# Kernel optimization log

Hardware: AMD Instinct MI355X
Metric: run time of the kernel (lower is better)

The kernel has to match this reference:

```python
import jax, jax.numpy as jnp
import numpy as np

B, N, C, H = 2, 2048, 1024, 16
D = C // H
SCALE = D ** -0.5


def setup_inputs() -> dict:
    key = jax.random.key(0)
    ks = jax.random.split(key, 4)
    s = 0.02
    return {
        "x": jax.random.normal(ks[0], (B, N, C), dtype=jnp.float32),
        "f": jax.random.normal(ks[1], (B, N, C), dtype=jnp.float32),
        "W_qkv": jax.random.normal(ks[2], (C, 3 * C), dtype=jnp.float32) * s,
        "W_proj": jax.random.normal(ks[3], (C, C), dtype=jnp.float32) * s,
        "b_proj": jnp.zeros((C,), dtype=jnp.float32),
    }


def reference(x, f, W_qkv, W_proj, b_proj):
    b, n, c = x.shape
    h, d = H, c // H
    # qkv projection -> (B,N,3,H,D) -> q,k,v each (B,H,N,D)
    qkv = (x @ W_qkv).reshape(b, n, 3, h, d)
    q = jnp.transpose(qkv[:, :, 0], (0, 2, 1, 3))
    k = jnp.transpose(qkv[:, :, 1], (0, 2, 1, 3))
    v = jnp.transpose(qkv[:, :, 2], (0, 2, 1, 3))
    # full NxN scores, faithful to the original manual MHA
    attn = jax.nn.softmax(jnp.einsum("bhqd,bhkd->bhqk", q, k) * SCALE, axis=-1)
    av = jnp.einsum("bhqk,bhkd->bhqd", attn, v)  # (B,H,N,D)
    # pre-residual output branch
    attn2gcn = jnp.transpose(av, (0, 2, 1, 3)).reshape(b, n, c)
    # residual fuse with f (reshaped per-head in torch; equivalent to flat add)
    fused = attn2gcn + f
    out = fused @ W_proj + b_proj
    return (out, attn2gcn)
```

## Files before the change

### kernel.cpp

```cpp
#include <hip/hip_runtime.h>
#include <hip/hip_bf16.h>

#define OUT1_OFF 4194304
#define QSCALE 0.1803368801111204f

typedef __attribute__((ext_vector_type(8))) short bf16x8;
typedef __attribute__((ext_vector_type(4))) float f32x4;

__device__ __forceinline__ unsigned short f2bf(float x) {
    unsigned u = __float_as_uint(x);
    u += 0x7FFFu + ((u >> 16) & 1u);
    return (unsigned short)(u >> 16);
}

__device__ __forceinline__ void gl2lds16(const unsigned short* g, unsigned short* l) {
    __builtin_amdgcn_global_load_lds(
        (const __attribute__((address_space(1))) unsigned int*)g,
        (__attribute__((address_space(3))) unsigned int*)l, 16, 0, 0);
}

__global__ __launch_bounds__(256) void cvt_bf16(const float* __restrict__ s,
                                                unsigned short* __restrict__ d, int n4) {
    int i = blockIdx.x * 256 + threadIdx.x;
    if (i >= n4) return;
    float4 v = reinterpret_cast<const float4*>(s)[i];
    ushort4 o = make_ushort4(f2bf(v.x), f2bf(v.y), f2bf(v.z), f2bf(v.w));
    reinterpret_cast<ushort4*>(d)[i] = o;
}

__global__ __launch_bounds__(256) void cvt_t(const float* __restrict__ in,
                                             unsigned short* __restrict__ out,
                                             int Kd, int Nd) {
    __shared__ float T[64][65];
    const int tid = threadIdx.x;
    const int r0 = blockIdx.y * 64, c0 = blockIdx.x * 64;
    const int tr = tid >> 3, tc = (tid & 7) * 8;
#pragma unroll
    for (int rr = 0; rr < 64; rr += 32) {
        const float4* p = reinterpret_cast<const float4*>(&in[(r0 + tr + rr) * Nd + c0 + tc]);
        float4 v0 = p[0], v1 = p[1];
        T[tr + rr][tc + 0] = v0.x; T[tr + rr][tc + 1] = v0.y;
        T[tr + rr][tc + 2] = v0.z; T[tr + rr][tc + 3] = v0.w;
        T[tr + rr][tc + 4] = v1.x; T[tr + rr][tc + 5] = v1.y;
        T[tr + rr][tc + 6] = v1.z; T[tr + rr][tc + 7] = v1.w;
    }
    __syncthreads();
#pragma unroll
    for (int rr = 0; rr < 64; rr += 32) {
        int orow = tr + rr;
        ushort4 o0 = make_ushort4(f2bf(T[tc + 0][orow]), f2bf(T[tc + 1][orow]),
                                  f2bf(T[tc + 2][orow]), f2bf(T[tc + 3][orow]));
        ushort4 o1 = make_ushort4(f2bf(T[tc + 4][orow]), f2bf(T[tc + 5][orow]),
                                  f2bf(T[tc + 6][orow]), f2bf(T[tc + 7][orow]));
        unsigned short* dst = &out[(c0 + orow) * Kd + r0 + tc];
        *reinterpret_cast<ushort4*>(dst) = o0;
        *reinterpret_cast<ushort4*>(dst + 4) = o1;
    }
}

__global__ __launch_bounds__(256) void gemm_qkv(const unsigned short* __restrict__ A,
                                                const unsigned short* __restrict__ Bt,
                                                unsigned short* __restrict__ qb,
                                                unsigned short* __restrict__ kb,
                                                unsigned short* __restrict__ vtb) {
    __shared__ __align__(16) unsigned short Sh[16384];
    unsigned short* As = Sh;
    unsigned short* Bs = Sh + 8192;
    const int tid = threadIdx.x;
    const int w = tid >> 6, lane = tid & 63, quad = lane >> 4, l15 = lane & 15;
    const int m0 = blockIdx.y * 128, n0 = blockIdx.x * 128;
    const int wm = (w & 1) * 64, wn = (w >> 1) * 64;
    const int sw = (l15 & 7) << 3;
    f32x4 acc[4][4] = {};
    for (int k0 = 0; k0 < 1024; k0 += 64) {
        __syncthreads();
#pragma unroll
        for (int t = 0; t < 4; ++t) {
            int c = t * 256 + tid;
            int row = c >> 3, jg = ((c & 7) ^ (row & 7)) * 8;
            gl2lds16(&A[(m0 + row) * 1024 + k0 + jg], &As[c * 8]);
            gl2lds16(&Bt[(n0 + row) * 1024 + k0 + jg], &Bs[c * 8]);
        }
        __syncthreads();
#pragma unroll
        for (int kk = 0; kk < 2; ++kk) {
            bf16x8 af[4], bfr[4];
#pragma unroll
            for (int i = 0; i < 4; ++i)
                af[i] = *reinterpret_cast<const bf16x8*>(
                    &As[(wm + i * 16 + l15) * 64 + ((((kk * 4 + quad) << 3) ^ sw))]);
#pragma unroll
            for (int j = 0; j < 4; ++j)
                bfr[j] = *reinterpret_cast<const bf16x8*>(
                    &Bs[(wn + j * 16 + l15) * 64 + ((((kk * 4 + quad) << 3) ^ sw))]);
#pragma unroll
            for (int i = 0; i < 4; ++i)
#pragma unroll
                for (int j = 0; j < 4; ++j)
                    acc[i][j] = __builtin_amdgcn_mfma_f32_16x16x32_bf16(af[i], bfr[j], acc[i][j], 0, 0, 0);
        }
    }
    const int nbase = n0 + wn;
    const int t = nbase >> 10;
    __syncthreads();
    if (t < 2) {
#pragma unroll
        for (int j = 0; j < 4; ++j) {
            int n = nbase + j * 16 + l15;
            int h = (n & 1023) >> 6, dd = n & 63;
#pragma unroll
            for (int i = 0; i < 4; ++i)
#pragma unroll
                for (int r = 0; r < 4; ++r) {
                    int m = m0 + wm + i * 16 + quad * 4 + r;
                    int b = m >> 11, tok = m & 2047;
                    float v = acc[i][j][r];
                    if (t == 0) qb[(((b * 16 + h) * 2048) + tok) * 64 + dd] = f2bf(v * QSCALE);
                    else        kb[(((b * 16 + h) * 2048) + tok) * 64 + dd] = f2bf(v);
                }
        }
    } else {
        unsigned short* scr = Sh + w * 4096;
        const int mb = m0 + wm;
        const int b = mb >> 11, kblk = (mb & 2047) >> 6;
        const int h = (nbase & 1023) >> 6;
#pragma unroll
        for (int i = 0; i < 4; ++i) {
            int slot0 = ((i & 2) << 4) | (quad << 3) | ((i & 1) << 2);
#pragma unroll
            for (int j = 0; j < 4; ++j) {
                unsigned short h0 = f2bf(acc[i][j][0]), h1 = f2bf(acc[i][j][1]);
                unsigned short h2 = f2bf(acc[i][j][2]), h3 = f2bf(acc[i][j][3]);
                uint2 pk = make_uint2((unsigned)h0 | ((unsigned)h1 << 16),
                                      (unsigned)h2 | ((unsigned)h3 << 16));
                *reinterpret_cast<uint2*>(&scr[(j * 16 + l15) * 64 + slot0]) = pk;
            }
        }
        asm volatile("s_waitcnt lgkmcnt(0)" ::: "memory");
        unsigned short* vtile = vtb + (((b * 16 + h) * 32) + kblk) * 4096;
#pragma unroll
        for (int p = 0; p < 8; ++p) {
            int idx = (p * 64 + lane) * 8;
            *reinterpret_cast<uint4*>(&vtile[idx]) = *reinterpret_cast<const uint4*>(&scr[idx]);
        }
    }
}

__global__ __launch_bounds__(256) void attn_kernel(const unsigned short* __restrict__ qb,
                                                   const unsigned short* __restrict__ kb,
                                                   const unsigned short* __restrict__ vtb,
                                                   const float* __restrict__ f,
                                                   float* __restrict__ attn2_out,
                                                   unsigned short* __restrict__ fusedb) {
    __shared__ __align__(16) unsigned short Ksw[2][4096];
    __shared__ __align__(16) unsigned short Vsw[2][4096];
    const int tid = threadIdx.x;
    const int w = tid >> 6, lane = tid & 63, quad = lane >> 4, l15 = lane & 15;
    const int bid = blockIdx.x;
    const int qtile = bid >> 5;
    const int bh = (bid & 7) * 4 + ((bid >> 3) & 3);
    const int q0 = qtile * 128 + w * 32;
    const unsigned short* qrl = &qb[(bh * 2048 + q0 + l15) * 64 + quad * 8];
    const unsigned short* qrh = &qb[(bh * 2048 + q0 + 16 + l15) * 64 + quad * 8];
    bf16x8 ql0 = *reinterpret_cast<const bf16x8*>(qrl);
    bf16x8 ql1 = *reinterpret_cast<const bf16x8*>(qrl + 32);
    bf16x8 qh0 = *reinterpret_cast<const bf16x8*>(qrh);
    bf16x8 qh1 = *reinterpret_cast<const bf16x8*>(qrh + 32);
    const unsigned short* kt0 = kb + bh * 131072;
    const unsigned short* vt0 = vtb + bh * 131072;
    const int c1 = tid, c2 = tid + 256;
    const int gu1 = (((c1 & ~7) | ((c1 & 7) ^ ((c1 >> 3) & 7))) << 3);
    const int gu2 = (((c2 & ~7) | ((c2 & 7) ^ ((c2 >> 3) & 7))) << 3);
    const int sw = (l15 & 7) << 3;
    f32x4 Olo[4] = {}, Ohi[4] = {};
    float sl = 0.f, sh = 0.f;

    gl2lds16(kt0 + gu1, &Ksw[0][c1 * 8]);
    gl2lds16(kt0 + gu2, &Ksw[0][c2 * 8]);
    gl2lds16(vt0 + gu1, &Vsw[0][c1 * 8]);
    gl2lds16(vt0 + gu2, &Vsw[0][c2 * 8]);

    int buf = 0;
    for (int it = 0; it < 32; ++it, buf ^= 1) {
        __syncthreads();
        if (it < 31) {
            int toff = (it + 1) * 4096;
            gl2lds16(kt0 + toff + gu1, &Ksw[buf ^ 1][c1 * 8]);
            gl2lds16(kt0 + toff + gu2, &Ksw[buf ^ 1][c2 * 8]);
            gl2lds16(vt0 + toff + gu1, &Vsw[buf ^ 1][c1 * 8]);
            gl2lds16(vt0 + toff + gu2, &Vsw[buf ^ 1][c2 * 8]);
        }
        f32x4 Tlo[4], Thi[4];
#pragma unroll
        for (int s = 0; s < 4; ++s) {
            int krow = (s * 16 + l15) * 64;
            bf16x8 k0 = *reinterpret_cast<const bf16x8*>(&Ksw[buf][krow + ((quad << 3) ^ sw)]);
            bf16x8 k1 = *reinterpret_cast<const bf16x8*>(&Ksw[buf][krow + (((quad + 4) << 3) ^ sw)]);
            f32x4 z = {};
            z = __builtin_amdgcn_mfma_f32_16x16x32_bf16(k0, ql0, z, 0, 0, 0);
            z = __builtin_amdgcn_mfma_f32_16x16x32_bf16(k1, ql1, z, 0, 0, 0);
            Tlo[s] = z;
            f32x4 z2 = {};
            z2 = __builtin_amdgcn_mfma_f32_16x16x32_bf16(k0, qh0, z2, 0, 0, 0);
            z2 = __builtin_amdgcn_mfma_f32_16x16x32_bf16(k1, qh1, z2, 0, 0, 0);
            Thi[s] = z2;
        }
        bf16x8 plo0, plo1, phi0, phi1;
        {
            float p[4][4];
#pragma unroll
            for (int s = 0; s < 4; ++s)
#pragma unroll
                for (int r = 0; r < 4; ++r) { p[s][r] = __builtin_amdgcn_exp2f(Tlo[s][r]); sl += p[s][r]; }
            uint4 u0, u1;
            u0.x = __builtin_amdgcn_perm(__float_as_uint(p[0][1]), __float_as_uint(p[0][0]), 0x07060302u);
            u0.y = __builtin_amdgcn_perm(__float_as_uint(p[0][3]), __float_as_uint(p[0][2]), 0x07060302u);
            u0.z = __builtin_amdgcn_perm(__float_as_uint(p[1][1]), __float_as_uint(p[1][0]), 0x07060302u);
            u0.w = __builtin_amdgcn_perm(__float_as_uint(p[1][3]), __float_as_uint(p[1][2]), 0x07060302u);
            u1.x = __builtin_amdgcn_perm(__float_as_uint(p[2][1]), __float_as_uint(p[2][0]), 0x07060302u);
            u1.y = __builtin_amdgcn_perm(__float_as_uint(p[2][3]), __float_as_uint(p[2][2]), 0x07060302u);
            u1.z = __builtin_amdgcn_perm(__float_as_uint(p[3][1]), __float_as_uint(p[3][0]), 0x07060302u);
            u1.w = __builtin_amdgcn_perm(__float_as_uint(p[3][3]), __float_as_uint(p[3][2]), 0x07060302u);
            plo0 = __builtin_bit_cast(bf16x8, u0);
            plo1 = __builtin_bit_cast(bf16x8, u1);
        }
        {
            float p[4][4];
#pragma unroll
            for (int s = 0; s < 4; ++s)
#pragma unroll
                for (int r = 0; r < 4; ++r) { p[s][r] = __builtin_amdgcn_exp2f(Thi[s][r]); sh += p[s][r]; }
            uint4 u0, u1;
            u0.x = __builtin_amdgcn_perm(__float_as_uint(p[0][1]), __float_as_uint(p[0][0]), 0x07060302u);
            u0.y = __builtin_amdgcn_perm(__float_as_uint(p[0][3]), __float_as_uint(p[0][2]), 0x07060302u);
            u0.z = __builtin_amdgcn_perm(__float_as_uint(p[1][1]), __float_as_uint(p[1][0]), 0x07060302u);
            u0.w = __builtin_amdgcn_perm(__float_as_uint(p[1][3]), __float_as_uint(p[1][2]), 0x07060302u);
            u1.x = __builtin_amdgcn_perm(__float_as_uint(p[2][1]), __float_as_uint(p[2][0]), 0x07060302u);
            u1.y = __builtin_amdgcn_perm(__float_as_uint(p[2][3]), __float_as_uint(p[2][2]), 0x07060302u);
            u1.z = __builtin_amdgcn_perm(__float_as_uint(p[3][1]), __float_as_uint(p[3][0]), 0x07060302u);
            u1.w = __builtin_amdgcn_perm(__float_as_uint(p[3][3]), __float_as_uint(p[3][2]), 0x07060302u);
            phi0 = __builtin_bit_cast(bf16x8, u0);
            phi1 = __builtin_bit_cast(bf16x8, u1);
        }
#pragma unroll
        for (int c4 = 0; c4 < 4; ++c4) {
            int vrow = (c4 * 16 + l15) * 64;
            bf16x8 v0 = *reinterpret_cast<const bf16x8*>(&Vsw[buf][vrow + ((quad << 3) ^ sw)]);
            bf16x8 v1 = *reinterpret_cast<const bf16x8*>(&Vsw[buf][vrow + (((quad + 4) << 3) ^ sw)]);
            Olo[c4] = __builtin_amdgcn_mfma_f32_16x16x32_bf16(plo0, v0, Olo[c4], 0, 0, 0);
            Olo[c4] = __builtin_amdgcn_mfma_f32_16x16x32_bf16(plo1, v1, Olo[c4], 0, 0, 0);
            Ohi[c4] = __builtin_amdgcn_mfma_f32_16x16x32_bf16(phi0, v0, Ohi[c4], 0, 0, 0);
            Ohi[c4] = __builtin_amdgcn_mfma_f32_16x16x32_bf16(phi1, v1, Ohi[c4], 0, 0, 0);
        }
    }
    sl += __shfl_xor(sl, 16);
    sl += __shfl_xor(sl, 32);
    sh += __shfl_xor(sh, 16);
    sh += __shfl_xor(sh, 32);
    const int b = bh >> 4, h = bh & 15;
#pragma unroll
    for (int r = 0; r < 4; ++r) {
        float invl = 1.f / __shfl(sl, quad * 4 + r, 16);
        float invh = 1.f / __shfl(sh, quad * 4 + r, 16);
        int tokl = q0 + quad * 4 + r;
        int basel = (b * 2048 + tokl) * 1024 + h * 64;
        int baseh = basel + 16 * 1024;
#pragma unroll
        for (int c4 = 0; c4 < 4; ++c4) {
            int col = c4 * 16 + l15;
            float ol = Olo[c4][r] * invl;
            float oh = Ohi[c4][r] * invh;
            attn2_out[basel + col] = ol;
            attn2_out[baseh + col] = oh;
            fusedb[basel + col] = f2bf(ol + f[basel + col]);
            fusedb[baseh + col] = f2bf(oh + f[baseh + col]);
        }
    }
}

__global__ __launch_bounds__(256) void gemm_proj(const unsigned short* __restrict__ A,
                                                 const unsigned short* __restrict__ Bt,
                                                 const float* __restrict__ bias,
                                                 float* __restrict__ out) {
    __shared__ __align__(16) unsigned short As[8192];
    __shared__ __align__(16) unsigned short Bs[4096];
    const int tid = threadIdx.x;
    const int w = tid >> 6, lane = tid & 63, quad = lane >> 4, l15 = lane & 15;
    const int m0 = blockIdx.y * 128, n0 = blockIdx.x * 64;
    const int wm = (w & 1) * 64, wn = (w >> 1) * 32;
    const int sw = (l15 & 7) << 3;
    f32x4 acc[4][2] = {};
    for (int k0 = 0; k0 < 1024; k0 += 64) {
        __syncthreads();
#pragma unroll
        for (int t = 0; t < 4; ++t) {
            int c = t * 256 + tid;
            int row = c >> 3, jg = ((c & 7) ^ (row & 7)) * 8;
            gl2lds16(&A[(m0 + row) * 1024 + k0 + jg], &As[c * 8]);
            if (t < 2) gl2lds16(&Bt[(n0 + row) * 1024 + k0 + jg], &Bs[c * 8]);
        }
        __syncthreads();
#pragma unroll
        for (int kk = 0; kk < 2; ++kk) {
            bf16x8 af[4], bfr[2];
#pragma unroll
            for (int i = 0; i < 4; ++i)
                af[i] = *reinterpret_cast<const bf16x8*>(
                    &As[(wm + i * 16 + l15) * 64 + ((((kk * 4 + quad) << 3) ^ sw))]);
#pragma unroll
            for (int j = 0; j < 2; ++j)
                bfr[j] = *reinterpret_cast<const bf16x8*>(
                    &Bs[(wn + j * 16 + l15) * 64 + ((((kk * 4 + quad) << 3) ^ sw))]);
#pragma unroll
            for (int i = 0; i < 4; ++i)
#pragma unroll
                for (int j = 0; j < 2; ++j)
                    acc[i][j] = __builtin_amdgcn_mfma_f32_16x16x32_bf16(af[i], bfr[j], acc[i][j], 0, 0, 0);
        }
    }
#pragma unroll
    for (int j = 0; j < 2; ++j) {
        int n = n0 + wn + j * 16 + l15;
        float bv = bias[n];
#pragma unroll
        for (int i = 0; i < 4; ++i)
#pragma unroll
            for (int r = 0; r < 4; ++r) {
                int m = m0 + wm + i * 16 + quad * 4 + r;
                out[m * 1024 + n] = acc[i][j][r] + bv;
            }
    }
}

extern "C" void kernel_launch(void* const* d_in, const int* in_sizes, int n_in,
                              void* d_out, int out_size, void* d_ws, size_t ws_size,
                              hipStream_t stream) {
    const float* x      = (const float*)d_in[0];
    const float* f      = (const float*)d_in[1];
    const float* W_qkv  = (const float*)d_in[2];
    const float* W_proj = (const float*)d_in[3];
    const float* b_proj = (const float*)d_in[4];
    float* out   = (float*)d_out;
    float* attn2 = out + OUT1_OFF;

    char* ws = (char*)d_ws;
    unsigned short* xb     = (unsigned short*)(ws);
    unsigned short* wqkvT  = (unsigned short*)(ws + 8388608);
    unsigned short* wprojT = (unsigned short*)(ws + 14680064);
    unsigned short* qb     = (unsigned short*)(ws + 16777216);
    unsigned short* kb     = (unsigned short*)(ws + 25165824);
    unsigned short* vtb    = (unsigned short*)(ws + 33554432);
    unsigned short* fusedb = (unsigned short*)(ws + 41943040);

    cvt_bf16<<<4096, 256, 0, stream>>>(x, xb, 1048576);
    cvt_t<<<dim3(48, 16), 256, 0, stream>>>(W_qkv, wqkvT, 1024, 3072);
    cvt_t<<<dim3(16, 16), 256, 0, stream>>>(W_proj, wprojT, 1024, 1024);
    gemm_qkv<<<dim3(24, 32), 256, 0, stream>>>(xb, wqkvT, qb, kb, vtb);
    attn_kernel<<<512, 256, 0, stream>>>(qb, kb, vtb, f, attn2, fusedb);
    gemm_proj<<<dim3(16, 32), 256, 0, stream>>>(fusedb, wprojT, b_proj, out);
}
```

Before: 207.7 us.

## Merge prep kernels, shrink attention and proj tiles, compute row sums via MFMA

Merges the three conversion kernels into one launch to cut launch overhead. The attention kernel now gives each wave 16 query rows instead of 32, doubling the grid to 1024 blocks for more parallelism. Its double-buffer loop is manually unrolled and the softmax denominator is summed with an MFMA against a ones vector instead of scalar adds and shuffles. The projection GEMM tile shrinks from 128x64 to 64x64 to double its block count, at the cost of reloading K/V and weight tiles more often and doing less work per block.

After: 199.9 us. 1.04x faster.

```diff
diff --git a/kernel.cpp b/kernel.cpp
--- a/kernel.cpp
+++ b/kernel.cpp
@@ -19,21 +19,26 @@
         (__attribute__((address_space(3))) unsigned int*)l, 16, 0, 0);
 }
 
-__global__ __launch_bounds__(256) void cvt_bf16(const float* __restrict__ s,
-                                                unsigned short* __restrict__ d, int n4) {
-    int i = blockIdx.x * 256 + threadIdx.x;
-    if (i >= n4) return;
-    float4 v = reinterpret_cast<const float4*>(s)[i];
-    ushort4 o = make_ushort4(f2bf(v.x), f2bf(v.y), f2bf(v.z), f2bf(v.w));
-    reinterpret_cast<ushort4*>(d)[i] = o;
-}
-
-__global__ __launch_bounds__(256) void cvt_t(const float* __restrict__ in,
-                                             unsigned short* __restrict__ out,
-                                             int Kd, int Nd) {
+__global__ __launch_bounds__(256) void prep(const float* __restrict__ x,
+                                            const float* __restrict__ Wqkv,
+                                            const float* __restrict__ Wproj,
+                                            unsigned short* __restrict__ xb,
+                                            unsigned short* __restrict__ wqkvT,
+                                            unsigned short* __restrict__ wprojT) {
     __shared__ float T[64][65];
-    const int tid = threadIdx.x;
-    const int r0 = blockIdx.y * 64, c0 = blockIdx.x * 64;
+    const int bid = blockIdx.x, tid = threadIdx.x;
+    if (bid < 4096) {
+        int i = bid * 256 + tid;
+        float4 v = reinterpret_cast<const float4*>(x)[i];
+        ushort4 o = make_ushort4(f2bf(v.x), f2bf(v.y), f2bf(v.z), f2bf(v.w));
+        reinterpret_cast<ushort4*>(xb)[i] = o;
+        return;
+    }
+    const float* in; unsigned short* out; int Nd, bx, by;
+    if (bid < 4864) { int t = bid - 4096; in = Wqkv;  out = wqkvT;  Nd = 3072; bx = t % 48; by = t / 48; }
+    else            { int t = bid - 4864; in = Wproj; out = wprojT; Nd = 1024; bx = t % 16; by = t / 16; }
+    const int Kd = 1024;
+    const int r0 = by * 64, c0 = bx * 64;
     const int tr = tid >> 3, tc = (tid & 7) * 8;
 #pragma unroll
     for (int rr = 0; rr < 64; rr += 32) {
@@ -156,124 +161,92 @@
     __shared__ __align__(16) unsigned short Vsw[2][4096];
     const int tid = threadIdx.x;
     const int w = tid >> 6, lane = tid & 63, quad = lane >> 4, l15 = lane & 15;
-    const int bid = blockIdx.x;
-    const int qtile = bid >> 5;
-    const int bh = (bid & 7) * 4 + ((bid >> 3) & 3);
-    const int q0 = qtile * 128 + w * 32;
-    const unsigned short* qrl = &qb[(bh * 2048 + q0 + l15) * 64 + quad * 8];
-    const unsigned short* qrh = &qb[(bh * 2048 + q0 + 16 + l15) * 64 + quad * 8];
-    bf16x8 ql0 = *reinterpret_cast<const bf16x8*>(qrl);
-    bf16x8 ql1 = *reinterpret_cast<const bf16x8*>(qrl + 32);
-    bf16x8 qh0 = *reinterpret_cast<const bf16x8*>(qrh);
-    bf16x8 qh1 = *reinterpret_cast<const bf16x8*>(qrh + 32);
+    const int bh = blockIdx.x;
+    const int q0 = blockIdx.y * 64 + w * 16;
+    const unsigned short* qr = &qb[(bh * 2048 + q0 + l15) * 64 + quad * 8];
+    bf16x8 ql0 = *reinterpret_cast<const bf16x8*>(qr);
+    bf16x8 ql1 = *reinterpret_cast<const bf16x8*>(qr + 32);
     const unsigned short* kt0 = kb + bh * 131072;
     const unsigned short* vt0 = vtb + bh * 131072;
     const int c1 = tid, c2 = tid + 256;
     const int gu1 = (((c1 & ~7) | ((c1 & 7) ^ ((c1 >> 3) & 7))) << 3);
     const int gu2 = (((c2 & ~7) | ((c2 & 7) ^ ((c2 >> 3) & 7))) << 3);
     const int sw = (l15 & 7) << 3;
-    f32x4 Olo[4] = {}, Ohi[4] = {};
-    float sl = 0.f, sh = 0.f;
-
-    gl2lds16(kt0 + gu1, &Ksw[0][c1 * 8]);
-    gl2lds16(kt0 + gu2, &Ksw[0][c2 * 8]);
-    gl2lds16(vt0 + gu1, &Vsw[0][c1 * 8]);
-    gl2lds16(vt0 + gu2, &Vsw[0][c2 * 8]);
-
-    int buf = 0;
-    for (int it = 0; it < 32; ++it, buf ^= 1) {
-        __syncthreads();
-        if (it < 31) {
-            int toff = (it + 1) * 4096;
-            gl2lds16(kt0 + toff + gu1, &Ksw[buf ^ 1][c1 * 8]);
-            gl2lds16(kt0 + toff + gu2, &Ksw[buf ^ 1][c2 * 8]);
-            gl2lds16(vt0 + toff + gu1, &Vsw[buf ^ 1][c1 * 8]);
-            gl2lds16(vt0 + toff + gu2, &Vsw[buf ^ 1][c2 * 8]);
-        }
-        f32x4 Tlo[4], Thi[4];
+    f32x4 O[4] = {};
+    f32x4 asum = {};
+    bf16x8 ones;
+#pragma unroll
+    for (int j = 0; j < 8; ++j) ones[j] = (short)0x3F80;
+
+#define STAGE(IT, BUF) do { int _toff = (IT) * 4096;                    \
+        gl2lds16(kt0 + _toff + gu1, &Ksw[BUF][c1 * 8]);                 \
+        gl2lds16(kt0 + _toff + gu2, &Ksw[BUF][c2 * 8]);                 \
+        gl2lds16(vt0 + _toff + gu1, &Vsw[BUF][c1 * 8]);                 \
+        gl2lds16(vt0 + _toff + gu2, &Vsw[BUF][c2 * 8]); } while (0)
+
+    auto body = [&](int buf) {
+        f32x4 T[4];
 #pragma unroll
         for (int s = 0; s < 4; ++s) {
-            int krow = (s * 16 + l15) * 64;
-            bf16x8 k0 = *reinterpret_cast<const bf16x8*>(&Ksw[buf][krow + ((quad << 3) ^ sw)]);
-            bf16x8 k1 = *reinterpret_cast<const bf16x8*>(&Ksw[buf][krow + (((quad + 4) << 3) ^ sw)]);
+            const unsigned short* kr = &Ksw[buf][(s * 16 + l15) * 64];
+            bf16x8 k0 = *reinterpret_cast<const bf16x8*>(&kr[(quad << 3) ^ sw]);
+            bf16x8 k1 = *reinterpret_cast<const bf16x8*>(&kr[((quad + 4) << 3) ^ sw]);
             f32x4 z = {};
             z = __builtin_amdgcn_mfma_f32_16x16x32_bf16(k0, ql0, z, 0, 0, 0);
             z = __builtin_amdgcn_mfma_f32_16x16x32_bf16(k1, ql1, z, 0, 0, 0);
-            Tlo[s] = z;
-            f32x4 z2 = {};
-            z2 = __builtin_amdgcn_mfma_f32_16x16x32_bf16(k0, qh0, z2, 0, 0, 0);
-            z2 = __builtin_amdgcn_mfma_f32_16x16x32_bf16(k1, qh1, z2, 0, 0, 0);
-            Thi[s] = z2;
-        }
-        bf16x8 plo0, plo1, phi0, phi1;
-        {
-            float p[4][4];
-#pragma unroll
-            for (int s = 0; s < 4; ++s)
-#pragma unroll
-                for (int r = 0; r < 4; ++r) { p[s][r] = __builtin_amdgcn_exp2f(Tlo[s][r]); sl += p[s][r]; }
-            uint4 u0, u1;
-            u0.x = __builtin_amdgcn_perm(__float_as_uint(p[0][1]), __float_as_uint(p[0][0]), 0x07060302u);
-            u0.y = __builtin_amdgcn_perm(__float_as_uint(p[0][3]), __float_as_uint(p[0][2]), 0x07060302u);
-            u0.z = __builtin_amdgcn_perm(__float_as_uint(p[1][1]), __float_as_uint(p[1][0]), 0x07060302u);
-            u0.w = __builtin_amdgcn_perm(__float_as_uint(p[1][3]), __float_as_uint(p[1][2]), 0x07060302u);
-            u1.x = __builtin_amdgcn_perm(__float_as_uint(p[2][1]), __float_as_uint(p[2][0]), 0x07060302u);
-            u1.y = __builtin_amdgcn_perm(__float_as_uint(p[2][3]), __float_as_uint(p[2][2]), 0x07060302u);
-            u1.z = __builtin_amdgcn_perm(__float_as_uint(p[3][1]), __float_as_uint(p[3][0]), 0x07060302u);
-            u1.w = __builtin_amdgcn_perm(__float_as_uint(p[3][3]), __float_as_uint(p[3][2]), 0x07060302u);
-            plo0 = __builtin_bit_cast(bf16x8, u0);
-            plo1 = __builtin_bit_cast(bf16x8, u1);
-        }
-        {
-            float p[4][4];
-#pragma unroll
-            for (int s = 0; s < 4; ++s)
-#pragma unroll
-                for (int r = 0; r < 4; ++r) { p[s][r] = __builtin_amdgcn_exp2f(Thi[s][r]); sh += p[s][r]; }
-            uint4 u0, u1;
-            u0.x = __builtin_amdgcn_perm(__float_as_uint(p[0][1]), __float_as_uint(p[0][0]), 0x07060302u);
-            u0.y = __builtin_amdgcn_perm(__float_as_uint(p[0][3]), __float_as_uint(p[0][2]), 0x07060302u);
-            u0.z = __builtin_amdgcn_perm(__float_as_uint(p[1][1]), __float_as_uint(p[1][0]), 0x07060302u);
-            u0.w = __builtin_amdgcn_perm(__float_as_uint(p[1][3]), __float_as_uint(p[1][2]), 0x07060302u);
-            u1.x = __builtin_amdgcn_perm(__float_as_uint(p[2][1]), __float_as_uint(p[2][0]), 0x07060302u);
-            u1.y = __builtin_amdgcn_perm(__float_as_uint(p[2][3]), __float_as_uint(p[2][2]), 0x07060302u);
-            u1.z = __builtin_amdgcn_perm(__float_as_uint(p[3][1]), __float_as_uint(p[3][0]), 0x07060302u);
-            u1.w = __builtin_amdgcn_perm(__float_as_uint(p[3][3]), __float_as_uint(p[3][2]), 0x07060302u);
-            phi0 = __builtin_bit_cast(bf16x8, u0);
-            phi1 = __builtin_bit_cast(bf16x8, u1);
-        }
+            T[s] = z;
+        }
+        float p[4][4];
+#pragma unroll
+        for (int s = 0; s < 4; ++s)
+#pragma unroll
+            for (int r = 0; r < 4; ++r) p[s][r] = __builtin_amdgcn_exp2f(T[s][r]);
+        uint4 u0, u1;
+        u0.x = __builtin_amdgcn_perm(__float_as_uint(p[0][1]), __float_as_uint(p[0][0]), 0x07060302u);
+        u0.y = __builtin_amdgcn_perm(__float_as_uint(p[0][3]), __float_as_uint(p[0][2]), 0x07060302u);
+        u0.z = __builtin_amdgcn_perm(__float_as_uint(p[1][1]), __float_as_uint(p[1][0]), 0x07060302u);
+        u0.w = __builtin_amdgcn_perm(__float_as_uint(p[1][3]), __float_as_uint(p[1][2]), 0x07060302u);
+        u1.x = __builtin_amdgcn_perm(__float_as_uint(p[2][1]), __float_as_uint(p[2][0]), 0x07060302u);
+        u1.y = __builtin_amdgcn_perm(__float_as_uint(p[2][3]), __float_as_uint(p[2][2]), 0x07060302u);
+        u1.z = __builtin_amdgcn_perm(__float_as_uint(p[3][1]), __float_as_uint(p[3][0]), 0x07060302u);
+        u1.w = __builtin_amdgcn_perm(__float_as_uint(p[3][3]), __float_as_uint(p[3][2]), 0x07060302u);
+        bf16x8 pa0 = __builtin_bit_cast(bf16x8, u0);
+        bf16x8 pa1 = __builtin_bit_cast(bf16x8, u1);
+        asum = __builtin_amdgcn_mfma_f32_16x16x32_bf16(pa0, ones, asum, 0, 0, 0);
+        asum = __builtin_amdgcn_mfma_f32_16x16x32_bf16(pa1, ones, asum, 0, 0, 0);
 #pragma unroll
         for (int c4 = 0; c4 < 4; ++c4) {
-            int vrow = (c4 * 16 + l15) * 64;
-            bf16x8 v0 = *reinterpret_cast<const bf16x8*>(&Vsw[buf][vrow + ((quad << 3) ^ sw)]);
-            bf16x8 v1 = *reinterpret_cast<const bf16x8*>(&Vsw[buf][vrow + (((quad + 4) << 3) ^ sw)]);
-            Olo[c4] = __builtin_amdgcn_mfma_f32_16x16x32_bf16(plo0, v0, Olo[c4], 0, 0, 0);
-            Olo[c4] = __builtin_amdgcn_mfma_f32_16x16x32_bf16(plo1, v1, Olo[c4], 0, 0, 0);
-            Ohi[c4] = __builtin_amdgcn_mfma_f32_16x16x32_bf16(phi0, v0, Ohi[c4], 0, 0, 0);
-            Ohi[c4] = __builtin_amdgcn_mfma_f32_16x16x32_bf16(phi1, v1, Ohi[c4], 0, 0, 0);
-        }
-    }
-    sl += __shfl_xor(sl, 16);
-    sl += __shfl_xor(sl, 32);
-    sh += __shfl_xor(sh, 16);
-    sh += __shfl_xor(sh, 32);
+            const unsigned short* vr = &Vsw[buf][(c4 * 16 + l15) * 64];
+            bf16x8 v0 = *reinterpret_cast<const bf16x8*>(&vr[(quad << 3) ^ sw]);
+            bf16x8 v1 = *reinterpret_cast<const bf16x8*>(&vr[((quad + 4) << 3) ^ sw]);
+            O[c4] = __builtin_amdgcn_mfma_f32_16x16x32_bf16(pa0, v0, O[c4], 0, 0, 0);
+            O[c4] = __builtin_amdgcn_mfma_f32_16x16x32_bf16(pa1, v1, O[c4], 0, 0, 0);
+        }
+    };
+
+    STAGE(0, 0);
+    for (int it = 0; it < 32; it += 2) {
+        __syncthreads();
+        STAGE(it + 1, 1);
+        body(0);
+        __syncthreads();
+        if (it + 2 < 32) STAGE(it + 2, 0);
+        body(1);
+    }
+#undef STAGE
+
     const int b = bh >> 4, h = bh & 15;
 #pragma unroll
     for (int r = 0; r < 4; ++r) {
-        float invl = 1.f / __shfl(sl, quad * 4 + r, 16);
-        float invh = 1.f / __shfl(sh, quad * 4 + r, 16);
-        int tokl = q0 + quad * 4 + r;
-        int basel = (b * 2048 + tokl) * 1024 + h * 64;
-        int baseh = basel + 16 * 1024;
+        float inv = 1.f / asum[r];
+        int tok = q0 + quad * 4 + r;
+        int base = (b * 2048 + tok) * 1024 + h * 64;
 #pragma unroll
         for (int c4 = 0; c4 < 4; ++c4) {
             int col = c4 * 16 + l15;
-            float ol = Olo[c4][r] * invl;
-            float oh = Ohi[c4][r] * invh;
-            attn2_out[basel + col] = ol;
-            attn2_out[baseh + col] = oh;
-            fusedb[basel + col] = f2bf(ol + f[basel + col]);
-            fusedb[baseh + col] = f2bf(oh + f[baseh + col]);
+            float o = O[c4][r] * inv;
+            attn2_out[base + col] = o;
+            fusedb[base + col] = f2bf(o + f[base + col]);
         }
     }
 }
@@ -282,29 +255,29 @@
                                                  const unsigned short* __restrict__ Bt,
                                                  const float* __restrict__ bias,
                                                  float* __restrict__ out) {
-    __shared__ __align__(16) unsigned short As[8192];
+    __shared__ __align__(16) unsigned short As[4096];
     __shared__ __align__(16) unsigned short Bs[4096];
     const int tid = threadIdx.x;
     const int w = tid >> 6, lane = tid & 63, quad = lane >> 4, l15 = lane & 15;
-    const int m0 = blockIdx.y * 128, n0 = blockIdx.x * 64;
-    const int wm = (w & 1) * 64, wn = (w >> 1) * 32;
+    const int m0 = blockIdx.y * 64, n0 = blockIdx.x * 64;
+    const int wm = (w & 1) * 32, wn = (w >> 1) * 32;
     const int sw = (l15 & 7) << 3;
-    f32x4 acc[4][2] = {};
+    f32x4 acc[2][2] = {};
     for (int k0 = 0; k0 < 1024; k0 += 64) {
         __syncthreads();
 #pragma unroll
-        for (int t = 0; t < 4; ++t) {
+        for (int t = 0; t < 2; ++t) {
             int c = t * 256 + tid;
             int row = c >> 3, jg = ((c & 7) ^ (row & 7)) * 8;
             gl2lds16(&A[(m0 + row) * 1024 + k0 + jg], &As[c * 8]);
-            if (t < 2) gl2lds16(&Bt[(n0 + row) * 1024 + k0 + jg], &Bs[c * 8]);
+            gl2lds16(&Bt[(n0 + row) * 1024 + k0 + jg], &Bs[c * 8]);
         }
         __syncthreads();
 #pragma unroll
         for (int kk = 0; kk < 2; ++kk) {
-            bf16x8 af[4], bfr[2];
-#pragma unroll
-            for (int i = 0; i < 4; ++i)
+            bf16x8 af[2], bfr[2];
+#pragma unroll
+            for (int i = 0; i < 2; ++i)
                 af[i] = *reinterpret_cast<const bf16x8*>(
                     &As[(wm + i * 16 + l15) * 64 + ((((kk * 4 + quad) << 3) ^ sw))]);
 #pragma unroll
@@ -312,7 +285,7 @@
                 bfr[j] = *reinterpret_cast<const bf16x8*>(
                     &Bs[(wn + j * 16 + l15) * 64 + ((((kk * 4 + quad) << 3) ^ sw))]);
 #pragma unroll
-            for (int i = 0; i < 4; ++i)
+            for (int i = 0; i < 2; ++i)
 #pragma unroll
                 for (int j = 0; j < 2; ++j)
                     acc[i][j] = __builtin_amdgcn_mfma_f32_16x16x32_bf16(af[i], bfr[j], acc[i][j], 0, 0, 0);
@@ -323,7 +296,7 @@
         int n = n0 + wn + j * 16 + l15;
         float bv = bias[n];
 #pragma unroll
-        for (int i = 0; i < 4; ++i)
+        for (int i = 0; i < 2; ++i)
 #pragma unroll
             for (int r = 0; r < 4; ++r) {
                 int m = m0 + wm + i * 16 + quad * 4 + r;
@@ -352,10 +325,8 @@
     unsigned short* vtb    = (unsigned short*)(ws + 33554432);
     unsigned short* fusedb = (unsigned short*)(ws + 41943040);
 
-    cvt_bf16<<<4096, 256, 0, stream>>>(x, xb, 1048576);
-    cvt_t<<<dim3(48, 16), 256, 0, stream>>>(W_qkv, wqkvT, 1024, 3072);
-    cvt_t<<<dim3(16, 16), 256, 0, stream>>>(W_proj, wprojT, 1024, 1024);
+    prep<<<5120, 256, 0, stream>>>(x, W_qkv, W_proj, xb, wqkvT, wprojT);
     gemm_qkv<<<dim3(24, 32), 256, 0, stream>>>(xb, wqkvT, qb, kb, vtb);
-    attn_kernel<<<512, 256, 0, stream>>>(qb, kb, vtb, f, attn2, fusedb);
-    gemm_proj<<<dim3(16, 32), 256, 0, stream>>>(fusedb, wprojT, b_proj, out);
-}
+    attn_kernel<<<dim3(32, 32), 256, 0, stream>>>(qb, kb, vtb, f, attn2, fusedb);
+    gemm_proj<<<dim3(16, 64), 256, 0, stream>>>(fusedb, wprojT, b_proj, out);
+}
```
